# Kernel optimization log

Measured on AMD Instinct MI355X. Metric: run time of the kernel, lower is better.

The kernel has to match this reference:

```python
import jax, jax.numpy as jnp
import numpy as np


def setup_inputs() -> dict:
    key = jax.random.key(0)
    x = jax.random.normal(key, (128, 256, 32, 32), dtype=jnp.float32)
    return {"x": x, "topk": 5}


def reference(x, topk):
    B = x.shape[0]
    flat = x.reshape(B, -1)                      # [B, N]
    _, idx = jax.lax.top_k(flat, topk)           # [B, k] indices into N
    out = jnp.zeros_like(flat)
    out = out.at[jnp.arange(B)[:, None], idx].set(1.0)
    return out.reshape(x.shape)
```

## Files before the change

kernel.cpp:

```cpp
#include <hip/hip_runtime.h>
#include <limits.h>
#include <math.h>
#include <stdint.h>

#define BROWS 128
#define NCOLS (256 * 32 * 32)
#define K 5
#define BPR 16
#define TPB 256
#define CHUNK (NCOLS / BPR)
#define F4T (CHUNK / 4 / TPB)
#define CAP 1024

#define T_FILTER 3.3f

typedef float v4f __attribute__((ext_vector_type(4)));

__device__ __forceinline__ uint64_t make_key(float f, uint32_t idx) {
    uint32_t u = __float_as_uint(f);
    u = (u & 0x80000000u) ? ~u : (u | 0x80000000u);
    return ((uint64_t)u << 32) | (uint32_t)(~idx);
}
__device__ __forceinline__ float key_val(uint64_t k) {
    uint32_t u = (uint32_t)(k >> 32);
    u = (u & 0x80000000u) ? (u ^ 0x80000000u) : ~u;
    return __uint_as_float(u);
}
__device__ __forceinline__ uint32_t key_idx(uint64_t k) { return ~(uint32_t)k; }

#define KEY_NEG_INF 0x007FFFFF00000000ULL

__device__ __forceinline__ void insert5(uint64_t (&key)[K], uint64_t c) {
    if (c > key[K - 1]) {
        key[K - 1] = c;
#pragma unroll
        for (int s = K - 1; s > 0; --s) {
            if (key[s] > key[s - 1]) {
                uint64_t t = key[s]; key[s] = key[s - 1]; key[s - 1] = t;
            }
        }
    }
}

__device__ __forceinline__ void wave_reduce5(uint64_t (&key)[K]) {
#pragma unroll
    for (int off = 1; off < 64; off <<= 1) {
        uint64_t ok[K];
#pragma unroll
        for (int k = 0; k < K; ++k)
            ok[k] = __shfl_xor((unsigned long long)key[k], off, 64);
#pragma unroll
        for (int k = 0; k < K; ++k) insert5(key, ok[k]);
    }
}

__global__ void wta_zerocnt(int* __restrict__ cnt) {
    if (threadIdx.x < BROWS) cnt[threadIdx.x] = 0;
}

__global__ __launch_bounds__(TPB) void wta_fillfilter(const float* __restrict__ x,
                                                      float* __restrict__ out,
                                                      int* __restrict__ cnt,
                                                      uint64_t* __restrict__ cand) {
    const int gb  = blockIdx.x;
    const int row = gb / BPR;
    const int blk = gb % BPR;
    const size_t base = (size_t)gb * CHUNK;
    const float4* __restrict__ x4 = (const float4*)(x + base);
    v4f* __restrict__ o4 = (v4f*)(out + base);
    const int t = threadIdx.x;
    const v4f z = {0.f, 0.f, 0.f, 0.f};

#pragma unroll
    for (int h = 0; h < 2; ++h) {
        float4 r[F4T / 2];
#pragma unroll
        for (int j = 0; j < F4T / 2; ++j)
            r[j] = x4[t + (h * (F4T / 2) + j) * TPB];
#pragma unroll
        for (int j = 0; j < F4T / 2; ++j)
            __builtin_nontemporal_store(z, &o4[t + (h * (F4T / 2) + j) * TPB]);
#pragma unroll
        for (int j = 0; j < F4T / 2; ++j) {
            const float4 d = r[j];
            const float m = fmaxf(fmaxf(d.x, d.y), fmaxf(d.z, d.w));
            if (m >= T_FILTER) {
                const uint32_t e = (uint32_t)blk * CHUNK +
                                   (uint32_t)(t + (h * (F4T / 2) + j) * TPB) * 4u;
                const float vs[4] = {d.x, d.y, d.z, d.w};
#pragma unroll
                for (int c = 0; c < 4; ++c) {
                    if (vs[c] >= T_FILTER) {
                        const int slot = atomicAdd(&cnt[row], 1);
                        if (slot < CAP) cand[row * CAP + slot] = make_key(vs[c], e + c);
                    }
                }
            }
        }
    }
}

__global__ __launch_bounds__(TPB) void wta_fallback(const float* __restrict__ x,
                                                    int* __restrict__ cnt,
                                                    uint64_t* __restrict__ cand) {
    const int row = blockIdx.x;
    const int n = cnt[row];
    if (n >= K && n <= CAP) return;

    const float4* __restrict__ x4 = (const float4*)(x + (size_t)row * NCOLS);
    const int t = threadIdx.x;

    uint64_t key[K];
#pragma unroll
    for (int k = 0; k < K; ++k) key[k] = KEY_NEG_INF;
    float vmin = -INFINITY;

    for (int i = t; i < NCOLS / 4; i += TPB) {
        const float4 d = x4[i];
        const float m = fmaxf(fmaxf(d.x, d.y), fmaxf(d.z, d.w));
        if (m >= vmin) {
            const uint32_t e = (uint32_t)i * 4u;
            insert5(key, make_key(d.x, e + 0));
            insert5(key, make_key(d.y, e + 1));
            insert5(key, make_key(d.z, e + 2));
            insert5(key, make_key(d.w, e + 3));
            vmin = key_val(key[K - 1]);
        }
    }

    wave_reduce5(key);

    __shared__ uint64_t sk[TPB / 64][K];
    const int wave = t >> 6, lane = t & 63;
    if (lane == 0) {
#pragma unroll
        for (int k = 0; k < K; ++k) sk[wave][k] = key[k];
    }
    __syncthreads();
    if (t == 0) {
#pragma unroll
        for (int w = 1; w < TPB / 64; ++w)
#pragma unroll
            for (int k = 0; k < K; ++k) insert5(key, sk[w][k]);
#pragma unroll
        for (int k = 0; k < K; ++k) cand[row * CAP + k] = key[k];
        cnt[row] = K;
    }
}

__global__ __launch_bounds__(64) void wta_final(const int* __restrict__ cnt,
                                                const uint64_t* __restrict__ cand,
                                                float* __restrict__ out) {
    const int row = blockIdx.x, lane = threadIdx.x;
    const int n = min(cnt[row], CAP);

    uint64_t key[K];
#pragma unroll
    for (int k = 0; k < K; ++k) key[k] = KEY_NEG_INF;
    for (int c = lane; c < n; c += 64) insert5(key, cand[row * CAP + c]);

    wave_reduce5(key);

    if (lane == 0) {
#pragma unroll
        for (int k = 0; k < K; ++k)
            if (key[k] != KEY_NEG_INF)
                out[(size_t)row * NCOLS + key_idx(key[k])] = 1.0f;
    }
}

extern "C" void kernel_launch(void* const* d_in, const int* in_sizes, int n_in,
                              void* d_out, int out_size, void* d_ws, size_t ws_size,
                              hipStream_t stream) {
    const float* x = (const float*)d_in[0];
    float* out = (float*)d_out;

    uint64_t* cand = (uint64_t*)d_ws;
    int* cnt = (int*)(cand + (size_t)BROWS * CAP);

    wta_zerocnt<<<1, 128, 0, stream>>>(cnt);
    wta_fillfilter<<<BROWS * BPR, TPB, 0, stream>>>(x, out, cnt, cand);
    wta_fallback<<<BROWS, TPB, 0, stream>>>(x, cnt, cand);
    wta_final<<<BROWS, 64, 0, stream>>>(cnt, cand, out);
}
```

Before: 271.8 us.

## Split fused zero-fill/filter kernel into separate filter and fill kernels

Splits the fused kernel into a read-only filter pass and a separate zero-fill kernel that writes the output with ordinary stores. The filter pass records a per-thread bitmask of float4s that pass the threshold and re-reads only those from memory, so it no longer keeps the loaded values in registers. The intent is to let streaming reads and writes each run at full bandwidth without contending, and to lower register pressure. The cost is one extra kernel launch and the loss of read/write overlap within a single pass.

```diff
diff --git a/kernel.cpp b/kernel.cpp
--- a/kernel.cpp
+++ b/kernel.cpp
@@ -12,9 +12,11 @@
 #define F4T (CHUNK / 4 / TPB)
 #define CAP 1024
 
+#define TOTAL_F4 ((size_t)BROWS * NCOLS / 4)
+#define FILLB 4096
+#define FILLF4 (TOTAL_F4 / FILLB / TPB)
+
 #define T_FILTER 3.3f
-
-typedef float v4f __attribute__((ext_vector_type(4)));
 
 __device__ __forceinline__ uint64_t make_key(float f, uint32_t idx) {
     uint32_t u = __float_as_uint(f);
@@ -58,46 +60,45 @@
     if (threadIdx.x < BROWS) cnt[threadIdx.x] = 0;
 }
 
-__global__ __launch_bounds__(TPB) void wta_fillfilter(const float* __restrict__ x,
-                                                      float* __restrict__ out,
-                                                      int* __restrict__ cnt,
-                                                      uint64_t* __restrict__ cand) {
+__global__ __launch_bounds__(TPB) void wta_filter(const float* __restrict__ x,
+                                                  int* __restrict__ cnt,
+                                                  uint64_t* __restrict__ cand) {
     const int gb  = blockIdx.x;
     const int row = gb / BPR;
     const int blk = gb % BPR;
-    const size_t base = (size_t)gb * CHUNK;
-    const float4* __restrict__ x4 = (const float4*)(x + base);
-    v4f* __restrict__ o4 = (v4f*)(out + base);
+    const float4* __restrict__ x4 = (const float4*)(x + (size_t)gb * CHUNK);
     const int t = threadIdx.x;
-    const v4f z = {0.f, 0.f, 0.f, 0.f};
 
+    uint32_t mask = 0;
 #pragma unroll
-    for (int h = 0; h < 2; ++h) {
-        float4 r[F4T / 2];
+    for (int i = 0; i < F4T; ++i) {
+        const float4 d = x4[t + i * TPB];
+        const float m = fmaxf(fmaxf(d.x, d.y), fmaxf(d.z, d.w));
+        mask |= (m >= T_FILTER ? 1u : 0u) << i;
+    }
+
+    while (mask) {
+        const int i = __builtin_ctz(mask);
+        mask &= mask - 1;
+        const float4 d = x4[t + i * TPB];
+        const uint32_t e = (uint32_t)blk * CHUNK + (uint32_t)(t + i * TPB) * 4u;
+        const float vs[4] = {d.x, d.y, d.z, d.w};
 #pragma unroll
-        for (int j = 0; j < F4T / 2; ++j)
-            r[j] = x4[t + (h * (F4T / 2) + j) * TPB];
-#pragma unroll
-        for (int j = 0; j < F4T / 2; ++j)
-            __builtin_nontemporal_store(z, &o4[t + (h * (F4T / 2) + j) * TPB]);
-#pragma unroll
-        for (int j = 0; j < F4T / 2; ++j) {
-            const float4 d = r[j];
-            const float m = fmaxf(fmaxf(d.x, d.y), fmaxf(d.z, d.w));
-            if (m >= T_FILTER) {
-                const uint32_t e = (uint32_t)blk * CHUNK +
-                                   (uint32_t)(t + (h * (F4T / 2) + j) * TPB) * 4u;
-                const float vs[4] = {d.x, d.y, d.z, d.w};
-#pragma unroll
-                for (int c = 0; c < 4; ++c) {
-                    if (vs[c] >= T_FILTER) {
-                        const int slot = atomicAdd(&cnt[row], 1);
-                        if (slot < CAP) cand[row * CAP + slot] = make_key(vs[c], e + c);
-                    }
-                }
+        for (int c = 0; c < 4; ++c) {
+            if (vs[c] >= T_FILTER) {
+                const int slot = atomicAdd(&cnt[row], 1);
+                if (slot < CAP) cand[row * CAP + slot] = make_key(vs[c], e + c);
             }
         }
     }
+}
+
+__global__ __launch_bounds__(TPB) void wta_fill(float4* __restrict__ o4) {
+    const size_t base = (size_t)blockIdx.x * (TPB * FILLF4) + threadIdx.x;
+    const float4 z = make_float4(0.f, 0.f, 0.f, 0.f);
+#pragma unroll
+    for (int i = 0; i < FILLF4; ++i)
+        o4[base + (size_t)i * TPB] = z;
 }
 
 __global__ __launch_bounds__(TPB) void wta_fallback(const float* __restrict__ x,
@@ -179,7 +180,8 @@
     int* cnt = (int*)(cand + (size_t)BROWS * CAP);
 
     wta_zerocnt<<<1, 128, 0, stream>>>(cnt);
-    wta_fillfilter<<<BROWS * BPR, TPB, 0, stream>>>(x, out, cnt, cand);
+    wta_filter<<<BROWS * BPR, TPB, 0, stream>>>(x, cnt, cand);
+    wta_fill<<<FILLB, TPB, 0, stream>>>((float4*)out);
     wta_fallback<<<BROWS, TPB, 0, stream>>>(x, cnt, cand);
     wta_final<<<BROWS, 64, 0, stream>>>(cnt, cand, out);
 }
```

After: 278.9 us. 2.6% more time.
